# Kernel optimization log

Hardware: AMD Instinct MI355X
Metric: run time of the kernel (lower is better)

The kernel has to match this reference:

```python
import jax, jax.numpy as jnp
import numpy as np

B, S, H, L, O = 128, 2048, 128, 2, 2  # batch, seq, hidden(=input), layers, output


def setup_inputs() -> dict:
    key = jax.random.key(0)
    k1, k2, k3, k4, k5 = jax.random.split(key, 5)
    std = 1.0 / np.sqrt(H)
    x_data = jax.random.normal(k1, (B, S, H), dtype=jnp.float32)
    x_length = jax.random.randint(k2, (B,), 0, S, dtype=jnp.int32)
    x_label = jax.random.uniform(k3, (B,), dtype=jnp.float32)
    # torch Linear layout: y = x @ W.T ; init uniform(-1/sqrt(H), 1/sqrt(H))
    Wx2h = jax.random.uniform(k4, (L, 2 * H, H), minval=-std, maxval=std, dtype=jnp.float32)
    Wfc = jax.random.uniform(k5, (L, O, H), minval=-std, maxval=std, dtype=jnp.float32)
    return {"x_data": x_data, "x_length": x_length, "x_label": x_label,
            "Wx2h": Wx2h, "Wfc": Wfc}


def reference(x_data, x_length, x_label, Wx2h, Wfc):
    Bn, Sn, Hn = x_data.shape
    Ln = Wx2h.shape[0]
    # valid-timestep mask: seq index < x_length[i]
    mask = (jnp.arange(Sn)[None, :] < x_length[:, None]).astype(x_data.dtype)  # [B,S]

    def step(carry, inp):
        S1, S2 = carry            # each [L,B,H]
        x_t, m_t = inp            # [B,H], [B]
        h = x_t
        out = None
        S1_new, S2_new = [], []
        for l in range(Ln):
            gate = h @ Wx2h[l].T                    # [B,2H]
            m1, m2 = jnp.split(gate, 2, axis=1)
            s1n = S1[l] + jnp.tanh(m1)
            s2n = S2[l] + jnp.tanh(m2)
            Fu = jax.nn.relu(s1n)
            h = (1.0 - Fu) * s2n + Fu * S2[l]       # hy
            out = jax.nn.softmax(h @ Wfc[l].T, axis=1)  # [B,O]
            S1_new.append(s1n)
            S2_new.append(s2n)
        loss_t = m_t * (x_label - jax.nn.sigmoid(out[:, 1])) ** 2  # [B]
        return (jnp.stack(S1_new), jnp.stack(S2_new)), loss_t

    S0 = jnp.zeros((Ln, Bn, Hn), x_data.dtype)
    xs = (jnp.swapaxes(x_data, 0, 1), mask.T)  # time-major [S,B,H], [S,B]
    _, losses = jax.lax.scan(step, (S0, S0), xs)
    return jnp.sum(losses)
```

## Files before the change

### kernel.cpp

```cpp
#include <hip/hip_runtime.h>

typedef __bf16 bf16;
typedef __bf16 bf16x8 __attribute__((ext_vector_type(8)));
typedef float floatx4 __attribute__((ext_vector_type(4)));

#define BATCH 128
#define SEQ   2048
#define HID   128
#define TWOH  256
#define CH    128
#define NCH   16
#define MTOT  (BATCH * SEQ)

__device__ __forceinline__ float fast_tanh(float x) {
    float e = __builtin_amdgcn_exp2f(2.88539008177793f * x);
    return 1.0f - 2.0f * __builtin_amdgcn_rcpf(e + 1.0f);
}
__device__ __forceinline__ float fast_sigmoid(float x) {
    return __builtin_amdgcn_rcpf(1.0f + __builtin_amdgcn_exp2f(-1.44269504088896f * x));
}

union PK4 { unsigned long long u; bf16 h[4]; };
union PK8 { uint4 u; bf16 h[8]; };

__global__ __launch_bounds__(256) void convert_w_k(const float* __restrict__ W,
                                                   bf16* __restrict__ Wb) {
    int i = blockIdx.x * 256 + threadIdx.x;
    float4 v = ((const float4*)W)[i];
    int R  = i >> 5;
    int k0 = (i & 31) << 2;
    int n  = R & 127;
    int g  = k0 >> 3;
    int j0 = k0 & 7;
    PK4 pk;
    pk.h[0] = (bf16)v.x; pk.h[1] = (bf16)v.y;
    pk.h[2] = (bf16)v.z; pk.h[3] = (bf16)v.w;
    *(unsigned long long*)&Wb[R * 128 + ((g ^ (n & 7)) << 3) + j0] = pk.u;
}

__device__ __forceinline__ void tile_prefix(const float g[4][4], float pref[4][4],
                                            float* stripe_tot, int quad, int l16) {
    float mibase = 0.f;
    #pragma unroll
    for (int mi = 0; mi < 4; ++mi) {
        float s0 = g[mi][0];
        float s1 = s0 + g[mi][1];
        float s2 = s1 + g[mi][2];
        float s3 = s2 + g[mi][3];
        float tot = s3, xq = tot;
        float t = __shfl_up(xq, 16);
        if (quad >= 1) xq += t;
        t = __shfl_up(xq, 32);
        if (quad >= 2) xq += t;
        float excl = mibase + xq - tot;
        pref[mi][0] = excl + s0;
        pref[mi][1] = excl + s1;
        pref[mi][2] = excl + s2;
        pref[mi][3] = excl + s3;
        mibase += __shfl(xq, 48 + l16);
    }
    *stripe_tot = mibase;
}

__device__ __forceinline__ void gemm_tile(const bf16* As, const bf16* Bs,
                                          floatx4 acc[4][2], int wr, int wc,
                                          int quad, int l16) {
    #pragma unroll
    for (int s = 0; s < 4; ++s) {
        int kg = s * 4 + quad;
        bf16x8 af[4], bfr[2];
        #pragma unroll
        for (int mi = 0; mi < 4; ++mi) {
            int r = wr * 64 + mi * 16 + l16;
            af[mi] = *(const bf16x8*)&As[r * 128 + ((kg ^ (r & 7)) << 3)];
        }
        #pragma unroll
        for (int ni = 0; ni < 2; ++ni) {
            int n = wc * 32 + ni * 16 + l16;
            bfr[ni] = *(const bf16x8*)&Bs[n * 128 + ((kg ^ (n & 7)) << 3)];
        }
        #pragma unroll
        for (int mi = 0; mi < 4; ++mi)
            #pragma unroll
            for (int ni = 0; ni < 2; ++ni)
                acc[mi][ni] = __builtin_amdgcn_mfma_f32_16x16x32_bf16(
                    af[mi], bfr[ni], acc[mi][ni], 0, 0, 0);
    }
}

__device__ __forceinline__ void load_T_half(const uint4* __restrict__ T, long blk,
                                            int half, int tid, float g2[2][4][4]) {
    #pragma unroll
    for (int mi = 0; mi < 4; ++mi) {
        PK8 p;
        p.u = T[((blk * 2 + half) * 4 + mi) * 512 + tid];
        #pragma unroll
        for (int rr = 0; rr < 4; ++rr) {
            g2[0][mi][rr] = (float)p.h[rr];
            g2[1][mi][rr] = (float)p.h[4 + rr];
        }
    }
}

__device__ __forceinline__ void store_T_half(uint4* __restrict__ T, long blk,
                                             int half, int tid, const float g2[2][4][4]) {
    #pragma unroll
    for (int mi = 0; mi < 4; ++mi) {
        PK8 p;
        #pragma unroll
        for (int rr = 0; rr < 4; ++rr) {
            p.h[rr]     = (bf16)g2[0][mi][rr];
            p.h[4 + rr] = (bf16)g2[1][mi][rr];
        }
        T[((blk * 2 + half) * 4 + mi) * 512 + tid] = p.u;
    }
}


__global__ __launch_bounds__(512, 4) void l0_k(const float* __restrict__ x,
                                               const bf16* __restrict__ Wbs,
                                               uint4* __restrict__ T,
                                               float* __restrict__ Pout,
                                               const int* __restrict__ xlen) {
    __shared__ bf16 As[128 * 128];
    __shared__ bf16 Bs[128 * 128];
    __shared__ float psum[512];

    const int tid  = threadIdx.x;
    const int lane = tid & 63;
    const int wid  = tid >> 6;
    const int wr   = wid >> 2;
    const int wc   = wid & 3;
    const int quad = lane >> 4;
    const int l16  = lane & 15;
    const long blk = blockIdx.x;
    const int  bb  = (int)(blk >> 4);
    const int  cc  = (int)(blk & 15);
    if ((cc << 7) >= xlen[bb]) return;

    const long rowBase = blk * 128;

    uint4 wv[4];
    {
        const uint4* W8 = (const uint4*)Wbs;
        #pragma unroll
        for (int it = 0; it < 4; ++it) wv[it] = W8[it * 512 + tid];
    }

    {
        const float4* A4 = (const float4*)(x + rowBase * HID);
        #pragma unroll
        for (int it = 0; it < 8; ++it) {
            int i  = it * 512 + tid;
            int r  = i >> 5;
            int c4 = i & 31;
            float4 v = A4[i];
            int g = c4 >> 1, hf = c4 & 1;
            PK4 pk;
            pk.h[0] = (bf16)v.x; pk.h[1] = (bf16)v.y;
            pk.h[2] = (bf16)v.z; pk.h[3] = (bf16)v.w;
            *(unsigned long long*)&As[r * 128 + ((g ^ (r & 7)) << 3) + (hf << 2)] = pk.u;
        }
    }

    #pragma unroll
    for (int it = 0; it < 4; ++it)
        *(uint4*)&Bs[(it * 512 + tid) * 8] = wv[it];

    {
        const uint4* W8 = (const uint4*)(Wbs + 128 * HID);
        #pragma unroll
        for (int it = 0; it < 4; ++it) wv[it] = W8[it * 512 + tid];
    }
    __syncthreads();

    #pragma unroll
    for (int half = 0; half < 2; ++half) {
        floatx4 acc[4][2];
        #pragma unroll
        for (int a = 0; a < 4; ++a)
            #pragma unroll
            for (int b2 = 0; b2 < 2; ++b2) acc[a][b2] = (floatx4){0.f, 0.f, 0.f, 0.f};

        gemm_tile(As, Bs, acc, wr, wc, quad, l16);

        if (half == 0) {
            __syncthreads();
            #pragma unroll
            for (int it = 0; it < 4; ++it)
                *(uint4*)&Bs[(it * 512 + tid) * 8] = wv[it];
        }

        float g2[2][4][4];
        #pragma unroll
        for (int mi = 0; mi < 4; ++mi)
            #pragma unroll
            for (int ni = 0; ni < 2; ++ni)
                #pragma unroll
                for (int rr = 0; rr < 4; ++rr)
                    g2[ni][mi][rr] = fast_tanh(acc[mi][ni][rr]);

        store_T_half(T, blk, half, tid, g2);

        #pragma unroll
        for (int ni = 0; ni < 2; ++ni) {
            float cs = 0.f;
            #pragma unroll
            for (int mi = 0; mi < 4; ++mi)
                #pragma unroll
                for (int rr = 0; rr < 4; ++rr) cs += g2[ni][mi][rr];
            cs += __shfl_xor(cs, 16);
            cs += __shfl_xor(cs, 32);
            if (quad == 0)
                psum[wr * 256 + half * 128 + wc * 32 + ni * 16 + l16] = cs;
        }

        if (half == 0) __syncthreads();
    }

    __syncthreads();
    if (tid < 256) Pout[(blk << 8) + tid] = psum[tid] + psum[256 + tid];
}

__global__ __launch_bounds__(512, 4) void l1_k(const bf16* __restrict__ Wb1s,
                                               uint4* __restrict__ T,
                                               const float* __restrict__ P0,
                                               float* __restrict__ Pout,
                                               const int* __restrict__ xlen) {
    __shared__ bf16 As[128 * 128];
    __shared__ bf16 Bs[128 * 128];
    __shared__ float offP[256];
    __shared__ float auxp[128];
    __shared__ float psum[512];

    const int tid  = threadIdx.x;
    const int lane = tid & 63;
    const int wid  = tid >> 6;
    const int wr   = wid >> 2;
    const int wc   = wid & 3;
    const int quad = lane >> 4;
    const int l16  = lane & 15;
    const long blk = blockIdx.x;
    const int  bb  = (int)(blk >> 4);
    const int  cc  = (int)(blk & 15);
    if ((cc << 7) >= xlen[bb]) return;

    uint4 wv[4];
    {
        const uint4* W8 = (const uint4*)Wb1s;
        #pragma unroll
        for (int it = 0; it < 4; ++it) wv[it] = W8[it * 512 + tid];
    }

    float pv = 0.f;
    if (tid < 256) {
        #pragma unroll
        for (int cp = 0; cp < NCH - 1; ++cp) {
            float v = P0[(((long)(bb * NCH + cp)) << 8) + tid];
            pv += (cp < cc) ? v : 0.f;
        }
    }

    float p1[2][4][4];

    {
        float g2[2][4][4];
        load_T_half(T, blk, 0, tid, g2);
        if (tid < 256) offP[tid] = pv;
        float pref[2][4][4], st[2];
        #pragma unroll
        for (int ni = 0; ni < 2; ++ni) {
            tile_prefix(g2[ni], pref[ni], &st[ni], quad, l16);
            if (wr == 0 && quad == 0) auxp[wc * 32 + ni * 16 + l16] = st[ni];
        }
        #pragma unroll
        for (int it = 0; it < 4; ++it)
            *(uint4*)&Bs[(it * 512 + tid) * 8] = wv[it];
        {
            const uint4* W8 = (const uint4*)(Wb1s + 128 * HID);
            #pragma unroll
            for (int it = 0; it < 4; ++it) wv[it] = W8[it * 512 + tid];
        }
        __syncthreads();
        #pragma unroll
        for (int ni = 0; ni < 2; ++ni) {
            int col = wc * 32 + ni * 16 + l16;
            float off = offP[col];
            if (wr) off += auxp[col];
            #pragma unroll
            for (int mi = 0; mi < 4; ++mi)
                #pragma unroll
                for (int rr = 0; rr < 4; ++rr)
                    p1[ni][mi][rr] = pref[ni][mi][rr] + off;
        }
    }
    __syncthreads();

    {
        float g2[2][4][4];
        load_T_half(T, blk, 1, tid, g2);
        float pref[2][4][4], st[2];
        #pragma unroll
        for (int ni = 0; ni < 2; ++ni) {
            tile_prefix(g2[ni], pref[ni], &st[ni], quad, l16);
            if (wr == 0 && quad == 0) auxp[wc * 32 + ni * 16 + l16] = st[ni];
        }
        __syncthreads();
        #pragma unroll
        for (int ni = 0; ni < 2; ++ni) {
            int col = wc * 32 + ni * 16 + l16;
            int gsw = col >> 3, rem = col & 7;
            float off = offP[128 + col];
            if (wr) off += auxp[col];
            #pragma unroll
            for (int mi = 0; mi < 4; ++mi)
                #pragma unroll
                for (int rr = 0; rr < 4; ++rr) {
                    int row = wr * 64 + mi * 16 + quad * 4 + rr;
                    float h = pref[ni][mi][rr] + off -
                              fmaxf(p1[ni][mi][rr], 0.f) * g2[ni][mi][rr];
                    As[row * 128 + ((gsw ^ (row & 7)) << 3) + rem] = (bf16)h;
                }
        }
    }
    __syncthreads();

    #pragma unroll
    for (int half = 0; half < 2; ++half) {
        floatx4 acc[4][2];
        #pragma unroll
        for (int a = 0; a < 4; ++a)
            #pragma unroll
            for (int b2 = 0; b2 < 2; ++b2) acc[a][b2] = (floatx4){0.f, 0.f, 0.f, 0.f};

        gemm_tile(As, Bs, acc, wr, wc, quad, l16);

        if (half == 0) {
            __syncthreads();
            #pragma unroll
            for (int it = 0; it < 4; ++it)
                *(uint4*)&Bs[(it * 512 + tid) * 8] = wv[it];
        }

        float g2[2][4][4];
        #pragma unroll
        for (int mi = 0; mi < 4; ++mi)
            #pragma unroll
            for (int ni = 0; ni < 2; ++ni)
                #pragma unroll
                for (int rr = 0; rr < 4; ++rr)
                    g2[ni][mi][rr] = fast_tanh(acc[mi][ni][rr]);

        store_T_half(T, blk, half, tid, g2);

        #pragma unroll
        for (int ni = 0; ni < 2; ++ni) {
            float cs = 0.f;
            #pragma unroll
            for (int mi = 0; mi < 4; ++mi)
                #pragma unroll
                for (int rr = 0; rr < 4; ++rr) cs += g2[ni][mi][rr];
            cs += __shfl_xor(cs, 16);
            cs += __shfl_xor(cs, 32);
            if (quad == 0)
                psum[wr * 256 + half * 128 + wc * 32 + ni * 16 + l16] = cs;
        }

        if (half == 0) __syncthreads();
    }

    __syncthreads();
    if (tid < 256) Pout[(blk << 8) + tid] = psum[tid] + psum[256 + tid];
}

__global__ __launch_bounds__(512, 4) void loss_k(const uint4* __restrict__ T,
                                                 const float* __restrict__ P1,
                                                 const float* __restrict__ Wfc,
                                                 const int* __restrict__ xlen,
                                                 const float* __restrict__ xlab,
                                                 float* __restrict__ out) {
    __shared__ float offP[256];
    __shared__ float auxp[128];
    __shared__ float zbuf[4][128][2];
    __shared__ float red[2];

    const int tid  = threadIdx.x;
    const int lane = tid & 63;
    const int wid  = tid >> 6;
    const int wr   = wid >> 2;
    const int wc   = wid & 3;
    const int quad = lane >> 4;
    const int l16  = lane & 15;
    const long blk = blockIdx.x;
    const int  bb  = (int)(blk >> 4);
    const int  cc  = (int)(blk & 15);
    if ((cc << 7) >= xlen[bb]) return;

    float pv = 0.f;
    if (tid < 256) {
        #pragma unroll
        for (int cp = 0; cp < NCH - 1; ++cp) {
            float v = P1[(((long)(bb * NCH + cp)) << 8) + tid];
            pv += (cp < cc) ? v : 0.f;
        }
    }

    float p1[2][4][4];

    {
        float g2[2][4][4];
        load_T_half(T, blk, 0, tid, g2);
        if (tid < 256) offP[tid] = pv;
        float pref[2][4][4], st[2];
        #pragma unroll
        for (int ni = 0; ni < 2; ++ni) {
            tile_prefix(g2[ni], pref[ni], &st[ni], quad, l16);
            if (wr == 0 && quad == 0) auxp[wc * 32 + ni * 16 + l16] = st[ni];
        }
        __syncthreads();
        #pragma unroll
        for (int ni = 0; ni < 2; ++ni) {
            int col = wc * 32 + ni * 16 + l16;
            float off = offP[col];
            if (wr) off += auxp[col];
            #pragma unroll
            for (int mi = 0; mi < 4; ++mi)
                #pragma unroll
                for (int rr = 0; rr < 4; ++rr)
                    p1[ni][mi][rr] = pref[ni][mi][rr] + off;
        }
    }
    __syncthreads();

    {
        float g2[2][4][4];
        load_T_half(T, blk, 1, tid, g2);
        float pref[2][4][4], st[2];
        #pragma unroll
        for (int ni = 0; ni < 2; ++ni) {
            tile_prefix(g2[ni], pref[ni], &st[ni], quad, l16);
            if (wr == 0 && quad == 0) auxp[wc * 32 + ni * 16 + l16] = st[ni];
        }
        __syncthreads();

        float w0[2], w1[2], off[2];
        #pragma unroll
        for (int ni = 0; ni < 2; ++ni) {
            int col = wc * 32 + ni * 16 + l16;
            w0[ni] = Wfc[2 * HID + col];
            w1[ni] = Wfc[3 * HID + col];
            off[ni] = offP[128 + col];
            if (wr) off[ni] += auxp[col];
        }
        #pragma unroll
        for (int mi = 0; mi < 4; ++mi)
            #pragma unroll
            for (int rr = 0; rr < 4; ++rr) {
                float z0 = 0.f, z1 = 0.f;
                #pragma unroll
                for (int ni = 0; ni < 2; ++ni) {
                    float h = pref[ni][mi][rr] + off[ni] -
                              fmaxf(p1[ni][mi][rr], 0.f) * g2[ni][mi][rr];
                    z0 += h * w0[ni];
                    z1 += h * w1[ni];
                }
                z0 += __shfl_xor(z0, 1); z1 += __shfl_xor(z1, 1);
                z0 += __shfl_xor(z0, 2); z1 += __shfl_xor(z1, 2);
                z0 += __shfl_xor(z0, 4); z1 += __shfl_xor(z1, 4);
                z0 += __shfl_xor(z0, 8); z1 += __shfl_xor(z1, 8);
                if (l16 == 0) {
                    int row = wr * 64 + mi * 16 + quad * 4 + rr;
                    zbuf[wc][row][0] = z0;
                    zbuf[wc][row][1] = z1;
                }
            }
    }

    __syncthreads();
    float lsum = 0.f;
    if (tid < 128) {
        int row = tid;
        float z0 = zbuf[0][row][0] + zbuf[1][row][0] + zbuf[2][row][0] + zbuf[3][row][0];
        float z1 = zbuf[0][row][1] + zbuf[1][row][1] + zbuf[2][row][1] + zbuf[3][row][1];
        float o1 = fast_sigmoid(z1 - z0);
        float sg = fast_sigmoid(o1);
        float d = xlab[bb] - sg;
        if (cc * CH + row < xlen[bb]) lsum = d * d;
        lsum += __shfl_xor(lsum, 1);
        lsum += __shfl_xor(lsum, 2);
        lsum += __shfl_xor(lsum, 4);
        lsum += __shfl_xor(lsum, 8);
        lsum += __shfl_xor(lsum, 16);
        lsum += __shfl_xor(lsum, 32);
        if (lane == 0) red[wid] = lsum;
    }
    __syncthreads();
    if (tid == 0) atomicAdd(out, red[0] + red[1]);
}

extern "C" void kernel_launch(void* const* d_in, const int* in_sizes, int n_in,
                              void* d_out, int out_size, void* d_ws, size_t ws_size,
                              hipStream_t stream) {
    const float* x    = (const float*)d_in[0];
    const int*   xlen = (const int*)d_in[1];
    const float* xlab = (const float*)d_in[2];
    const float* Wx2h = (const float*)d_in[3];
    const float* Wfc  = (const float*)d_in[4];
    float* out = (float*)d_out;

    char* ws = (char*)d_ws;
    uint4* T  = (uint4*)ws;
    float* P0 = (float*)(ws + (size_t)MTOT * TWOH * 2);
    float* P1 = P0 + (size_t)BATCH * NCH * TWOH;
    bf16*  Wb = (bf16*)(P1 + (size_t)BATCH * NCH * TWOH);

    hipMemsetAsync(d_out, 0, sizeof(float), stream);
    convert_w_k<<<64, 256, 0, stream>>>(Wx2h, Wb);

    l0_k<<<MTOT / 128, 512, 0, stream>>>(x, Wb, T, P0, xlen);
    l1_k<<<MTOT / 128, 512, 0, stream>>>(Wb + (size_t)TWOH * HID, T, P0, P1, xlen);
    loss_k<<<MTOT / 128, 512, 0, stream>>>(T, P1, Wfc, xlen, xlab, out);
}
```

Before: 355.5 us.

## Load layer-0 A fragments directly from global and prefetch T halves early

In l0_k the input tile is no longer staged through LDS; each wave loads fp32 rows straight from global, converts them to bf16 in registers, and double-buffers the fragments across the k-steps. In l1_k and loss_k both halves of T are loaded early into registers. The aux buffer is split in two so one barrier between the halves can be dropped. The aim is to cut LDS traffic, shared memory use and barrier stalls, and to hide global latency. The cost is more registers and A reads from global that are strided and not coalesced, with each row read by several waves.

```diff
diff --git a/kernel.cpp b/kernel.cpp
--- a/kernel.cpp
+++ b/kernel.cpp
@@ -21,7 +21,7 @@
 }
 
 union PK4 { unsigned long long u; bf16 h[4]; };
-union PK8 { uint4 u; bf16 h[8]; };
+union PK8 { uint4 u; bf16 h[8]; bf16x8 v; };
 
 __global__ __launch_bounds__(256) void convert_w_k(const float* __restrict__ W,
                                                    bf16* __restrict__ Wb) {
@@ -62,6 +62,15 @@
     *stripe_tot = mibase;
 }
 
+__device__ __forceinline__ bf16x8 ldAf(const float* __restrict__ p) {
+    float4 a0 = *(const float4*)p;
+    float4 a1 = *(const float4*)(p + 4);
+    bf16x8 r;
+    r[0] = (bf16)a0.x; r[1] = (bf16)a0.y; r[2] = (bf16)a0.z; r[3] = (bf16)a0.w;
+    r[4] = (bf16)a1.x; r[5] = (bf16)a1.y; r[6] = (bf16)a1.z; r[7] = (bf16)a1.w;
+    return r;
+}
+
 __device__ __forceinline__ void gemm_tile(const bf16* As, const bf16* Bs,
                                           floatx4 acc[4][2], int wr, int wc,
                                           int quad, int l16) {
@@ -88,12 +97,11 @@
     }
 }
 
-__device__ __forceinline__ void load_T_half(const uint4* __restrict__ T, long blk,
-                                            int half, int tid, float g2[2][4][4]) {
+__device__ __forceinline__ void decode_T(const uint4 tr[4], float g2[2][4][4]) {
     #pragma unroll
     for (int mi = 0; mi < 4; ++mi) {
         PK8 p;
-        p.u = T[((blk * 2 + half) * 4 + mi) * 512 + tid];
+        p.u = tr[mi];
         #pragma unroll
         for (int rr = 0; rr < 4; ++rr) {
             g2[0][mi][rr] = (float)p.h[rr];
@@ -122,7 +130,6 @@
                                                uint4* __restrict__ T,
                                                float* __restrict__ Pout,
                                                const int* __restrict__ xlen) {
-    __shared__ bf16 As[128 * 128];
     __shared__ bf16 Bs[128 * 128];
     __shared__ float psum[512];
 
@@ -138,39 +145,19 @@
     const int  cc  = (int)(blk & 15);
     if ((cc << 7) >= xlen[bb]) return;
 
-    const long rowBase = blk * 128;
+    const float* ab = x + ((size_t)blk * 128 + (size_t)(wr * 64 + l16)) * HID;
 
     uint4 wv[4];
     {
         const uint4* W8 = (const uint4*)Wbs;
         #pragma unroll
         for (int it = 0; it < 4; ++it) wv[it] = W8[it * 512 + tid];
-    }
-
-    {
-        const float4* A4 = (const float4*)(x + rowBase * HID);
-        #pragma unroll
-        for (int it = 0; it < 8; ++it) {
-            int i  = it * 512 + tid;
-            int r  = i >> 5;
-            int c4 = i & 31;
-            float4 v = A4[i];
-            int g = c4 >> 1, hf = c4 & 1;
-            PK4 pk;
-            pk.h[0] = (bf16)v.x; pk.h[1] = (bf16)v.y;
-            pk.h[2] = (bf16)v.z; pk.h[3] = (bf16)v.w;
-            *(unsigned long long*)&As[r * 128 + ((g ^ (r & 7)) << 3) + (hf << 2)] = pk.u;
-        }
-    }
-
-    #pragma unroll
-    for (int it = 0; it < 4; ++it)
-        *(uint4*)&Bs[(it * 512 + tid) * 8] = wv[it];
-
-    {
-        const uint4* W8 = (const uint4*)(Wbs + 128 * HID);
-        #pragma unroll
-        for (int it = 0; it < 4; ++it) wv[it] = W8[it * 512 + tid];
+        #pragma unroll
+        for (int it = 0; it < 4; ++it)
+            *(uint4*)&Bs[(it * 512 + tid) * 8] = wv[it];
+        const uint4* W81 = (const uint4*)(Wbs + 128 * HID);
+        #pragma unroll
+        for (int it = 0; it < 4; ++it) wv[it] = W81[it * 512 + tid];
     }
     __syncthreads();
 
@@ -182,7 +169,32 @@
             #pragma unroll
             for (int b2 = 0; b2 < 2; ++b2) acc[a][b2] = (floatx4){0.f, 0.f, 0.f, 0.f};
 
-        gemm_tile(As, Bs, acc, wr, wc, quad, l16);
+        bf16x8 af2[2][4];
+        #pragma unroll
+        for (int mi = 0; mi < 4; ++mi)
+            af2[0][mi] = ldAf(ab + (size_t)mi * 16 * HID + quad * 8);
+        #pragma unroll
+        for (int s = 0; s < 4; ++s) {
+            int kg = s * 4 + quad;
+            if (s < 3) {
+                #pragma unroll
+                for (int mi = 0; mi < 4; ++mi)
+                    af2[(s + 1) & 1][mi] =
+                        ldAf(ab + (size_t)mi * 16 * HID + (kg + 4) * 8);
+            }
+            bf16x8 bfr[2];
+            #pragma unroll
+            for (int ni = 0; ni < 2; ++ni) {
+                int n = wc * 32 + ni * 16 + l16;
+                bfr[ni] = *(const bf16x8*)&Bs[n * 128 + ((kg ^ (n & 7)) << 3)];
+            }
+            #pragma unroll
+            for (int mi = 0; mi < 4; ++mi)
+                #pragma unroll
+                for (int ni = 0; ni < 2; ++ni)
+                    acc[mi][ni] = __builtin_amdgcn_mfma_f32_16x16x32_bf16(
+                        af2[s & 1][mi], bfr[ni], acc[mi][ni], 0, 0, 0);
+        }
 
         if (half == 0) {
             __syncthreads();
@@ -230,7 +242,7 @@
     __shared__ bf16 As[128 * 128];
     __shared__ bf16 Bs[128 * 128];
     __shared__ float offP[256];
-    __shared__ float auxp[128];
+    __shared__ float aux[2][128];
     __shared__ float psum[512];
 
     const int tid  = threadIdx.x;
@@ -251,6 +263,9 @@
         #pragma unroll
         for (int it = 0; it < 4; ++it) wv[it] = W8[it * 512 + tid];
     }
+    uint4 tr[4];
+    #pragma unroll
+    for (int mi = 0; mi < 4; ++mi) tr[mi] = T[((blk * 2 + 0) * 4 + mi) * 512 + tid];
 
     float pv = 0.f;
     if (tid < 256) {
@@ -261,67 +276,64 @@
         }
     }
 
+    float g2[2][4][4];
+    decode_T(tr, g2);
+    #pragma unroll
+    for (int mi = 0; mi < 4; ++mi) tr[mi] = T[((blk * 2 + 1) * 4 + mi) * 512 + tid];
+
+    float pref[2][4][4], st[2];
+    #pragma unroll
+    for (int ni = 0; ni < 2; ++ni) {
+        tile_prefix(g2[ni], pref[ni], &st[ni], quad, l16);
+        if (wr == 0 && quad == 0) aux[0][wc * 32 + ni * 16 + l16] = st[ni];
+    }
+    #pragma unroll
+    for (int it = 0; it < 4; ++it)
+        *(uint4*)&Bs[(it * 512 + tid) * 8] = wv[it];
+    {
+        const uint4* W8 = (const uint4*)(Wb1s + 128 * HID);
+        #pragma unroll
+        for (int it = 0; it < 4; ++it) wv[it] = W8[it * 512 + tid];
+    }
+    if (tid < 256) offP[tid] = pv;
+    __syncthreads();
+
     float p1[2][4][4];
-
-    {
-        float g2[2][4][4];
-        load_T_half(T, blk, 0, tid, g2);
-        if (tid < 256) offP[tid] = pv;
-        float pref[2][4][4], st[2];
-        #pragma unroll
-        for (int ni = 0; ni < 2; ++ni) {
-            tile_prefix(g2[ni], pref[ni], &st[ni], quad, l16);
-            if (wr == 0 && quad == 0) auxp[wc * 32 + ni * 16 + l16] = st[ni];
-        }
-        #pragma unroll
-        for (int it = 0; it < 4; ++it)
-            *(uint4*)&Bs[(it * 512 + tid) * 8] = wv[it];
-        {
-            const uint4* W8 = (const uint4*)(Wb1s + 128 * HID);
-            #pragma unroll
-            for (int it = 0; it < 4; ++it) wv[it] = W8[it * 512 + tid];
-        }
-        __syncthreads();
-        #pragma unroll
-        for (int ni = 0; ni < 2; ++ni) {
-            int col = wc * 32 + ni * 16 + l16;
-            float off = offP[col];
-            if (wr) off += auxp[col];
-            #pragma unroll
-            for (int mi = 0; mi < 4; ++mi)
-                #pragma unroll
-                for (int rr = 0; rr < 4; ++rr)
-                    p1[ni][mi][rr] = pref[ni][mi][rr] + off;
-        }
-    }
-    __syncthreads();
-
-    {
-        float g2[2][4][4];
-        load_T_half(T, blk, 1, tid, g2);
-        float pref[2][4][4], st[2];
-        #pragma unroll
-        for (int ni = 0; ni < 2; ++ni) {
-            tile_prefix(g2[ni], pref[ni], &st[ni], quad, l16);
-            if (wr == 0 && quad == 0) auxp[wc * 32 + ni * 16 + l16] = st[ni];
-        }
-        __syncthreads();
-        #pragma unroll
-        for (int ni = 0; ni < 2; ++ni) {
-            int col = wc * 32 + ni * 16 + l16;
-            int gsw = col >> 3, rem = col & 7;
-            float off = offP[128 + col];
-            if (wr) off += auxp[col];
-            #pragma unroll
-            for (int mi = 0; mi < 4; ++mi)
-                #pragma unroll
-                for (int rr = 0; rr < 4; ++rr) {
-                    int row = wr * 64 + mi * 16 + quad * 4 + rr;
-                    float h = pref[ni][mi][rr] + off -
-                              fmaxf(p1[ni][mi][rr], 0.f) * g2[ni][mi][rr];
-                    As[row * 128 + ((gsw ^ (row & 7)) << 3) + rem] = (bf16)h;
-                }
-        }
+    #pragma unroll
+    for (int ni = 0; ni < 2; ++ni) {
+        int col = wc * 32 + ni * 16 + l16;
+        float off = offP[col];
+        if (wr) off += aux[0][col];
+        #pragma unroll
+        for (int mi = 0; mi < 4; ++mi)
+            #pragma unroll
+            for (int rr = 0; rr < 4; ++rr)
+                p1[ni][mi][rr] = pref[ni][mi][rr] + off;
+    }
+
+    decode_T(tr, g2);
+    #pragma unroll
+    for (int ni = 0; ni < 2; ++ni) {
+        tile_prefix(g2[ni], pref[ni], &st[ni], quad, l16);
+        if (wr == 0 && quad == 0) aux[1][wc * 32 + ni * 16 + l16] = st[ni];
+    }
+    __syncthreads();
+
+    #pragma unroll
+    for (int ni = 0; ni < 2; ++ni) {
+        int col = wc * 32 + ni * 16 + l16;
+        int gsw = col >> 3, rem = col & 7;
+        float off = offP[128 + col];
+        if (wr) off += aux[1][col];
+        #pragma unroll
+        for (int mi = 0; mi < 4; ++mi)
+            #pragma unroll
+            for (int rr = 0; rr < 4; ++rr) {
+                int row = wr * 64 + mi * 16 + quad * 4 + rr;
+                float h = pref[ni][mi][rr] + off -
+                          fmaxf(p1[ni][mi][rr], 0.f) * g2[ni][mi][rr];
+                As[row * 128 + ((gsw ^ (row & 7)) << 3) + rem] = (bf16)h;
+            }
     }
     __syncthreads();
 
@@ -342,16 +354,16 @@
                 *(uint4*)&Bs[(it * 512 + tid) * 8] = wv[it];
         }
 
-        float g2[2][4][4];
+        float g2h[2][4][4];
         #pragma unroll
         for (int mi = 0; mi < 4; ++mi)
             #pragma unroll
             for (int ni = 0; ni < 2; ++ni)
                 #pragma unroll
                 for (int rr = 0; rr < 4; ++rr)
-                    g2[ni][mi][rr] = fast_tanh(acc[mi][ni][rr]);
-
-        store_T_half(T, blk, half, tid, g2);
+                    g2h[ni][mi][rr] = fast_tanh(acc[mi][ni][rr]);
+
+        store_T_half(T, blk, half, tid, g2h);
 
         #pragma unroll
         for (int ni = 0; ni < 2; ++ni) {
@@ -359,7 +371,7 @@
             #pragma unroll
             for (int mi = 0; mi < 4; ++mi)
                 #pragma unroll
-                for (int rr = 0; rr < 4; ++rr) cs += g2[ni][mi][rr];
+                for (int rr = 0; rr < 4; ++rr) cs += g2h[ni][mi][rr];
             cs += __shfl_xor(cs, 16);
             cs += __shfl_xor(cs, 32);
             if (quad == 0)
@@ -380,7 +392,7 @@
                                                  const float* __restrict__ xlab,
                                                  float* __restrict__ out) {
     __shared__ float offP[256];
-    __shared__ float auxp[128];
+    __shared__ float aux[2][128];
     __shared__ float zbuf[4][128][2];
     __shared__ float red[2];
 
@@ -396,6 +408,10 @@
     const int  cc  = (int)(blk & 15);
     if ((cc << 7) >= xlen[bb]) return;
 
+    uint4 tr[4];
+    #pragma unroll
+    for (int mi = 0; mi < 4; ++mi) tr[mi] = T[((blk * 2 + 0) * 4 + mi) * 512 + tid];
+
     float pv = 0.f;
     if (tid < 256) {
         #pragma unroll
@@ -405,44 +421,42 @@
         }
     }
 
+    float g2[2][4][4];
+    decode_T(tr, g2);
+    #pragma unroll
+    for (int mi = 0; mi < 4; ++mi) tr[mi] = T[((blk * 2 + 1) * 4 + mi) * 512 + tid];
+
+    float pref[2][4][4], st[2];
+    #pragma unroll
+    for (int ni = 0; ni < 2; ++ni) {
+        tile_prefix(g2[ni], pref[ni], &st[ni], quad, l16);
+        if (wr == 0 && quad == 0) aux[0][wc * 32 + ni * 16 + l16] = st[ni];
+    }
+    if (tid < 256) offP[tid] = pv;
+    __syncthreads();
+
     float p1[2][4][4];
+    #pragma unroll
+    for (int ni = 0; ni < 2; ++ni) {
+        int col = wc * 32 + ni * 16 + l16;
+        float off = offP[col];
+        if (wr) off += aux[0][col];
+        #pragma unroll
+        for (int mi = 0; mi < 4; ++mi)
+            #pragma unroll
+            for (int rr = 0; rr < 4; ++rr)
+                p1[ni][mi][rr] = pref[ni][mi][rr] + off;
+    }
+
+    decode_T(tr, g2);
+    #pragma unroll
+    for (int ni = 0; ni < 2; ++ni) {
+        tile_prefix(g2[ni], pref[ni], &st[ni], quad, l16);
+        if (wr == 0 && quad == 0) aux[1][wc * 32 + ni * 16 + l16] = st[ni];
+    }
+    __syncthreads();
 
     {
-        float g2[2][4][4];
-        load_T_half(T, blk, 0, tid, g2);
-        if (tid < 256) offP[tid] = pv;
-        float pref[2][4][4], st[2];
-        #pragma unroll
-        for (int ni = 0; ni < 2; ++ni) {
-            tile_prefix(g2[ni], pref[ni], &st[ni], quad, l16);
-            if (wr == 0 && quad == 0) auxp[wc * 32 + ni * 16 + l16] = st[ni];
-        }
-        __syncthreads();
-        #pragma unroll
-        for (int ni = 0; ni < 2; ++ni) {
-            int col = wc * 32 + ni * 16 + l16;
-            float off = offP[col];
-            if (wr) off += auxp[col];
-            #pragma unroll
-            for (int mi = 0; mi < 4; ++mi)
-                #pragma unroll
-                for (int rr = 0; rr < 4; ++rr)
-                    p1[ni][mi][rr] = pref[ni][mi][rr] + off;
-        }
-    }
-    __syncthreads();
-
-    {
-        float g2[2][4][4];
-        load_T_half(T, blk, 1, tid, g2);
-        float pref[2][4][4], st[2];
-        #pragma unroll
-        for (int ni = 0; ni < 2; ++ni) {
-            tile_prefix(g2[ni], pref[ni], &st[ni], quad, l16);
-            if (wr == 0 && quad == 0) auxp[wc * 32 + ni * 16 + l16] = st[ni];
-        }
-        __syncthreads();
-
         float w0[2], w1[2], off[2];
         #pragma unroll
         for (int ni = 0; ni < 2; ++ni) {
@@ -450,7 +464,7 @@
             w0[ni] = Wfc[2 * HID + col];
             w1[ni] = Wfc[3 * HID + col];
             off[ni] = offP[128 + col];
-            if (wr) off[ni] += auxp[col];
+            if (wr) off[ni] += aux[1][col];
         }
         #pragma unroll
         for (int mi = 0; mi < 4; ++mi)
```

After: 418.1 us. 17.6% more time.
